# Kernel optimization log

Hardware: AMD Instinct MI355X
Metric: run time of the kernel (lower is better)

The kernel has to match this reference:

```python
import jax, jax.numpy as jnp
import numpy as np

# MX microscaling decode helpers. Codes are stored as int32 holding uint8 bit patterns.
_FP4_MAG = jnp.array([0.0, 0.5, 1.0, 1.5, 2.0, 3.0, 4.0, 6.0], dtype=jnp.float32)  # E2M1

def dec_fp4(c):
    # c in [0,16): bit3 = sign, bits0-2 index E2M1 magnitude LUT
    s = jnp.where(c >= 8, -1.0, 1.0)
    return s * _FP4_MAG[c & 7]

def dec_fp6(c):
    # E3M2, bias 3. bit5 sign, bits2-4 exp, bits0-1 mantissa
    s = jnp.where(c >= 32, -1.0, 1.0)
    e = ((c >> 2) & 7).astype(jnp.float32)
    m = (c & 3).astype(jnp.float32)
    mag = jnp.where(e == 0, m * 0.25 * 0.25, (1.0 + m * 0.25) * jnp.exp2(e - 3.0))
    return s * mag

def dec_fp8(c):
    # E4M3, bias 7. bit7 sign, bits3-6 exp, bits0-2 mantissa (NaN code decoded as 480, consistent both sides)
    s = jnp.where(c >= 128, -1.0, 1.0)
    e = ((c >> 3) & 15).astype(jnp.float32)
    m = (c & 7).astype(jnp.float32)
    mag = jnp.where(e == 0, m * 0.125 * jnp.exp2(-6.0), (1.0 + m * 0.125) * jnp.exp2(e - 7.0))
    return s * mag

def unpack4(p):
    # [..., K//2] bytes -> [..., K] nibbles; low nibble = even element, high = odd
    lo = p & 15
    hi = (p >> 4) & 15
    return jnp.stack([lo, hi], axis=-1).reshape(*p.shape[:-1], p.shape[-1] * 2)

def unpack6(p):
    # little-endian 6-bit packing: 4 values per 3 bytes. [..., K*6//8] -> [..., K]
    g = p.reshape(*p.shape[:-1], -1, 3)
    b0, b1, b2 = g[..., 0], g[..., 1], g[..., 2]
    v0 = b0 & 0x3F
    v1 = ((b0 >> 6) & 3) | ((b1 & 0x0F) << 2)
    v2 = ((b1 >> 4) & 0x0F) | ((b2 & 3) << 4)
    v3 = (b2 >> 2) & 0x3F
    return jnp.stack([v0, v1, v2, v3], axis=-1).reshape(*p.shape[:-1], p.shape[-1] * 4 // 3)

def blockscale(x, sf):
    # x [..., K] fp32, sf [..., K//32] E8M0 exponents: scale = 2^(sf-127) per 32-element block
    scale = jnp.exp2(sf.astype(jnp.float32) - 127.0)
    xs = x.reshape(*x.shape[:-1], -1, 32) * scale[..., None]
    return xs.reshape(x.shape)

def dequant(codes, sf, bits):
    if bits == 4:
        x = dec_fp4(unpack4(codes))
    elif bits == 6:
        x = dec_fp6(unpack6(codes))
    else:
        x = dec_fp8(codes)
    return blockscale(x, sf)


def setup_inputs() -> dict:
    key = jax.random.key(0)
    ks = jax.random.split(key, 13)
    M, N = 4096, 4096
    p4, p6, p8 = 3072, 768, 256
    ri = lambda k, sh: jax.random.randint(k, sh, 0, 256, dtype=jnp.int32)
    sf = lambda k, sh: jax.random.randint(k, sh, 121, 132, dtype=jnp.int32)
    return {
        "AN": ri(ks[0], (M, p4 // 2)),
        "AS": ri(ks[1], (M, p6 * 6 // 8)),
        "AO": ri(ks[2], (M, p8)),
        "SFAN": sf(ks[3], (M, p4 // 32)),
        "SFAS": sf(ks[4], (M, p6 // 32)),
        "SFAO": sf(ks[5], (M, p8 // 32)),
        "BN": ri(ks[6], (N, p4 // 2)),
        "BS": ri(ks[7], (N, p6 * 6 // 8)),
        "BO": ri(ks[8], (N, p8)),
        "SFBN": sf(ks[9], (N * p4 // 32,)),
        "SFBS": sf(ks[10], (N * p6 // 32,)),
        "SFBO": sf(ks[11], (N * p8 // 32,)),
        "bias": jax.random.normal(ks[12], (N,), dtype=jnp.float32) * 0.02,
    }


def reference(AN, AS, AO, SFAN, SFAS, SFAO, BN, BS, BO, SFBN, SFBS, SFBO, bias):
    N = BN.shape[0]
    a4 = dequant(AN, SFAN, 4)                       # [M, p4]
    w4 = dequant(BN, SFBN.reshape(N, -1), 4)        # [N, p4]
    a6 = dequant(AS, SFAS, 6)                       # [M, p6]
    w6 = dequant(BS, SFBS.reshape(N, -1), 6)        # [N, p6]
    a8 = dequant(AO, SFAO, 8)                       # [M, p8]
    w8 = dequant(BO, SFBO.reshape(N, -1), 8)        # [N, p8]
    y = a4 @ w4.T + a6 @ w6.T + a8 @ w8.T           # [M, N]
    return y + bias
```

## Files before the change

kernel.cpp:

```cpp
#include <hip/hip_runtime.h>

typedef short short8 __attribute__((ext_vector_type(8)));
typedef int   intx8  __attribute__((ext_vector_type(8)));
typedef float floatx16 __attribute__((ext_vector_type(16)));

__device__ __forceinline__ unsigned pk4(int a, int b, int c, int d) {
    return (a & 255) | ((b & 255) << 8) | ((c & 255) << 16) | ((unsigned)(d & 255) << 24);
}

__device__ __forceinline__ unsigned dec8bf(int c, int esf) {
    int s = (c & 128) << 8;
    int e = (c >> 3) & 15, m = c & 7;
    int rn = s | ((e + 120 + esf) << 7) | (m << 4);
    int nb = (m >= 4) ? 2 : ((m >= 2) ? 1 : 0);
    int rs = m ? (s | ((nb + 118 + esf) << 7) | ((m << (7 - nb)) & 0x7F)) : s;
    return (unsigned)(e ? rn : rs);
}

__device__ __forceinline__ void pack_one(
    int t, const int* __restrict__ Pn, const int* __restrict__ Ps, const int* __restrict__ Po,
    const int* __restrict__ Sn, const int* __restrict__ Ss, const int* __restrict__ So,
    unsigned char* __restrict__ C4, unsigned char* __restrict__ C6,
    unsigned short* __restrict__ C8, unsigned char* __restrict__ St, int R)
{
    int T0 = R * 384, T1 = T0 + R * 144, T2 = T1 + R * 64, T3 = T2 + R * 24, T4 = T3 + R * 12;
    if (t < T0) {
        int r = t / 384, i = t - r * 384;
        int4 b = *(const int4*)(Pn + (size_t)r * 1536 + i * 4);
        *(unsigned*)(C4 + ((size_t)(i >> 2) * R + r) * 16 + (i & 3) * 4) = pk4(b.x, b.y, b.z, b.w);
    } else if (t < T1) {
        t -= T0; int r = t / 144, i = t - r * 144;
        int4 b = *(const int4*)(Ps + (size_t)r * 576 + i * 4);
        *(unsigned*)(C6 + ((size_t)(i / 6) * R + r) * 24 + (i % 6) * 4) = pk4(b.x, b.y, b.z, b.w);
    } else if (t < T2) {
        t -= T1; int r = t / 64, i = t - r * 64;
        int4 c = *(const int4*)(Po + (size_t)r * 256 + i * 4);
        int e = So[r * 8 + (i >> 3)] - 127;
        unsigned lo = dec8bf(c.x & 255, e) | (dec8bf(c.y & 255, e) << 16);
        unsigned hi = dec8bf(c.z & 255, e) | (dec8bf(c.w & 255, e) << 16);
        *(int2*)((unsigned char*)C8 + ((size_t)(i >> 1) * R + r) * 16 + (i & 1) * 8) =
            (int2){ (int)lo, (int)hi };
    } else if (t < T3) {
        t -= T2; int r = t / 24, q = t - r * 24;
        int4 v = *(const int4*)(Sn + (size_t)r * 96 + q * 4);
        *(unsigned*)(St + ((size_t)q * R + r) * 4) = pk4(v.x, v.y, v.z, v.w);
    } else if (t < T4) {
        t -= T3; int r = t / 12, b2 = t - r * 12;
        int2 sp = *(const int2*)(Ss + (size_t)r * 24 + 2 * b2);
        *(unsigned*)(St + ((size_t)(24 + b2) * R + r) * 4) =
            (unsigned)((sp.x & 255) | ((sp.y & 255) << 8));
    }
}

__global__ __launch_bounds__(256) void pack_both(
    const int* __restrict__ AN, const int* __restrict__ AS, const int* __restrict__ AO,
    const int* __restrict__ SAn, const int* __restrict__ SAs, const int* __restrict__ SAo,
    unsigned char* __restrict__ A4, unsigned char* __restrict__ A6,
    unsigned short* __restrict__ A8, unsigned char* __restrict__ SaT, int M,
    const int* __restrict__ BN, const int* __restrict__ BS, const int* __restrict__ BO,
    const int* __restrict__ SBn, const int* __restrict__ SBs, const int* __restrict__ SBo,
    unsigned char* __restrict__ B4, unsigned char* __restrict__ B6,
    unsigned short* __restrict__ B8, unsigned char* __restrict__ SbT, int N)
{
    int t = blockIdx.x * 256 + threadIdx.x;
    int TA = M * 628;
    if (t < TA) pack_one(t, AN, AS, AO, SAn, SAs, SAo, A4, A6, A8, SaT, M);
    else        pack_one(t - TA, BN, BS, BO, SBn, SBs, SBo, B4, B6, B8, SbT, N);
}

__global__ __launch_bounds__(256, 3) void gemm_mx(
    const unsigned char* __restrict__ A4, const unsigned char* __restrict__ B4,
    const unsigned char* __restrict__ A6, const unsigned char* __restrict__ B6,
    const unsigned short* __restrict__ A8, const unsigned short* __restrict__ B8,
    const unsigned char* __restrict__ SaT, const unsigned char* __restrict__ SbT,
    const float* __restrict__ bias, float* __restrict__ C, int M, int N)
{
    int tid = threadIdx.x, w = tid >> 6, l = tid & 63;
    int nbm = M >> 7, nbn = N >> 7;
    int bm, bn;
    if (nbm == 32 && nbn == 32) {
        int o = blockIdx.y * 32 + blockIdx.x;
        int xcd = o & 7, pos = o >> 3;
        int tile = pos >> 4, idx = pos & 15;
        bm = xcd * 4 + (idx & 3);
        bn = tile * 4 + (idx >> 2);
    } else { bm = blockIdx.y; bn = blockIdx.x; }

    int wm = (w >> 1) * 64, wn = (w & 1) * 64;
    int lr = l & 31, lh = l >> 5;

    floatx16 acc[2][2] = {};

    int rA[2] = { bm * 128 + wm + lr, bm * 128 + wm + 32 + lr };
    int cB[2] = { bn * 128 + wn + lr, bn * 128 + wn + 32 + lr };

    {
        unsigned strA = 32u * (unsigned)M, strB = 32u * (unsigned)N;
        unsigned fA0 = ((unsigned)lh * M + (unsigned)rA[0]) * 16u;
        unsigned fA1 = ((unsigned)lh * M + (unsigned)rA[1]) * 16u;
        unsigned fB0 = ((unsigned)lh * N + (unsigned)cB[0]) * 16u;
        unsigned fB1 = ((unsigned)lh * N + (unsigned)cB[1]) * 16u;

        int4 pa[3][2], pb[3][2];
        #pragma unroll
        for (int s = 0; s < 3; ++s) {
            pa[s][0] = *(const int4*)(A4 + fA0); pa[s][1] = *(const int4*)(A4 + fA1);
            pb[s][0] = *(const int4*)(B4 + fB0); pb[s][1] = *(const int4*)(B4 + fB1);
            fA0 += strA; fA1 += strA; fB0 += strB; fB1 += strB;
        }

        unsigned sstrA = 4u * (unsigned)M, sstrB = 4u * (unsigned)N;
        unsigned sA0 = (unsigned)rA[0] * 4u, sA1 = (unsigned)rA[1] * 4u;
        unsigned sB0 = (unsigned)cB[0] * 4u, sB1 = (unsigned)cB[1] * 4u;
        unsigned psa[2][2], psb[2][2];
        psa[0][0] = *(const unsigned*)(SaT + sA0);         psa[0][1] = *(const unsigned*)(SaT + sA1);
        psb[0][0] = *(const unsigned*)(SbT + sB0);         psb[0][1] = *(const unsigned*)(SbT + sB1);
        psa[1][0] = *(const unsigned*)(SaT + sA0 + sstrA); psa[1][1] = *(const unsigned*)(SaT + sA1 + sstrA);
        psb[1][0] = *(const unsigned*)(SbT + sB0 + sstrB); psb[1][1] = *(const unsigned*)(SbT + sB1 + sstrB);
        sA0 += 2 * sstrA; sA1 += 2 * sstrA; sB0 += 2 * sstrB; sB1 += 2 * sstrB;

        #pragma unroll 12
        for (int u = 0; u < 48; ++u) {
            int sl = u % 3, wsl = (u >> 1) & 1;
            int sh = 8 * ((u & 1) * 2 + lh);
            int sa0 = (int)((psa[wsl][0] >> sh) & 255), sa1 = (int)((psa[wsl][1] >> sh) & 255);
            int sb0 = (int)((psb[wsl][0] >> sh) & 255), sb1 = (int)((psb[wsl][1] >> sh) & 255);
            intx8 A0 = (intx8){ pa[sl][0].x, pa[sl][0].y, pa[sl][0].z, pa[sl][0].w, 0, 0, 0, 0 };
            intx8 A1 = (intx8){ pa[sl][1].x, pa[sl][1].y, pa[sl][1].z, pa[sl][1].w, 0, 0, 0, 0 };
            intx8 B0 = (intx8){ pb[sl][0].x, pb[sl][0].y, pb[sl][0].z, pb[sl][0].w, 0, 0, 0, 0 };
            intx8 B1 = (intx8){ pb[sl][1].x, pb[sl][1].y, pb[sl][1].z, pb[sl][1].w, 0, 0, 0, 0 };
            acc[0][0] = __builtin_amdgcn_mfma_scale_f32_32x32x64_f8f6f4(A0, B0, acc[0][0], 4, 4, 0, sa0, 0, sb0);
            acc[0][1] = __builtin_amdgcn_mfma_scale_f32_32x32x64_f8f6f4(A0, B1, acc[0][1], 4, 4, 0, sa0, 0, sb1);
            acc[1][0] = __builtin_amdgcn_mfma_scale_f32_32x32x64_f8f6f4(A1, B0, acc[1][0], 4, 4, 0, sa1, 0, sb0);
            acc[1][1] = __builtin_amdgcn_mfma_scale_f32_32x32x64_f8f6f4(A1, B1, acc[1][1], 4, 4, 0, sa1, 0, sb1);
            pa[sl][0] = *(const int4*)(A4 + fA0); pa[sl][1] = *(const int4*)(A4 + fA1);
            pb[sl][0] = *(const int4*)(B4 + fB0); pb[sl][1] = *(const int4*)(B4 + fB1);
            fA0 += strA; fA1 += strA; fB0 += strB; fB1 += strB;
            if (u & 1) {
                psa[wsl][0] = *(const unsigned*)(SaT + sA0); psa[wsl][1] = *(const unsigned*)(SaT + sA1);
                psb[wsl][0] = *(const unsigned*)(SbT + sB0); psb[wsl][1] = *(const unsigned*)(SbT + sB1);
                sA0 += sstrA; sA1 += sstrA; sB0 += sstrB; sB1 += sstrB;
            }
        }
    }

    {
        unsigned str6A = 48u * (unsigned)M, str6B = 48u * (unsigned)N;
        unsigned gA0 = ((unsigned)lh * M + (unsigned)rA[0]) * 24u;
        unsigned gA1 = ((unsigned)lh * M + (unsigned)rA[1]) * 24u;
        unsigned gB0 = ((unsigned)lh * N + (unsigned)cB[0]) * 24u;
        unsigned gB1 = ((unsigned)lh * N + (unsigned)cB[1]) * 24u;
        unsigned ss4A = 4u * (unsigned)M, ss4B = 4u * (unsigned)N;
        unsigned zA0 = (24u * (unsigned)M + (unsigned)rA[0]) * 4u;
        unsigned zA1 = (24u * (unsigned)M + (unsigned)rA[1]) * 4u;
        unsigned zB0 = (24u * (unsigned)N + (unsigned)cB[0]) * 4u;
        unsigned zB1 = (24u * (unsigned)N + (unsigned)cB[1]) * 4u;

        int2 qa[2][2][3], qb[2][2][3];
        unsigned p6a[2][2], p6b[2][2];
        #pragma unroll
        for (int s = 0; s < 2; ++s) {
            const unsigned char *a0 = A6 + gA0, *a1 = A6 + gA1, *b0 = B6 + gB0, *b1 = B6 + gB1;
            qa[s][0][0] = *(const int2*)(a0); qa[s][0][1] = *(const int2*)(a0 + 8); qa[s][0][2] = *(const int2*)(a0 + 16);
            qa[s][1][0] = *(const int2*)(a1); qa[s][1][1] = *(const int2*)(a1 + 8); qa[s][1][2] = *(const int2*)(a1 + 16);
            qb[s][0][0] = *(const int2*)(b0); qb[s][0][1] = *(const int2*)(b0 + 8); qb[s][0][2] = *(const int2*)(b0 + 16);
            qb[s][1][0] = *(const int2*)(b1); qb[s][1][1] = *(const int2*)(b1 + 8); qb[s][1][2] = *(const int2*)(b1 + 16);
            p6a[s][0] = *(const unsigned*)(SaT + zA0); p6a[s][1] = *(const unsigned*)(SaT + zA1);
            p6b[s][0] = *(const unsigned*)(SbT + zB0); p6b[s][1] = *(const unsigned*)(SbT + zB1);
            gA0 += str6A; gA1 += str6A; gB0 += str6B; gB1 += str6B;
            zA0 += ss4A; zA1 += ss4A; zB0 += ss4B; zB1 += ss4B;
        }
        int sh6 = 8 * lh;
        #pragma unroll 2
        for (int v = 0; v < 10; ++v) {
            int sl = v & 1;
            int sa0 = (int)((p6a[sl][0] >> sh6) & 255), sa1 = (int)((p6a[sl][1] >> sh6) & 255);
            int sb0 = (int)((p6b[sl][0] >> sh6) & 255), sb1 = (int)((p6b[sl][1] >> sh6) & 255);
            intx8 A0 = (intx8){ qa[sl][0][0].x, qa[sl][0][0].y, qa[sl][0][1].x, qa[sl][0][1].y, qa[sl][0][2].x, qa[sl][0][2].y, 0, 0 };
            intx8 A1 = (intx8){ qa[sl][1][0].x, qa[sl][1][0].y, qa[sl][1][1].x, qa[sl][1][1].y, qa[sl][1][2].x, qa[sl][1][2].y, 0, 0 };
            intx8 B0 = (intx8){ qb[sl][0][0].x, qb[sl][0][0].y, qb[sl][0][1].x, qb[sl][0][1].y, qb[sl][0][2].x, qb[sl][0][2].y, 0, 0 };
            intx8 B1 = (intx8){ qb[sl][1][0].x, qb[sl][1][0].y, qb[sl][1][1].x, qb[sl][1][1].y, qb[sl][1][2].x, qb[sl][1][2].y, 0, 0 };
            acc[0][0] = __builtin_amdgcn_mfma_scale_f32_32x32x64_f8f6f4(A0, B0, acc[0][0], 3, 3, 0, sa0, 0, sb0);
            acc[0][1] = __builtin_amdgcn_mfma_scale_f32_32x32x64_f8f6f4(A0, B1, acc[0][1], 3, 3, 0, sa0, 0, sb1);
            acc[1][0] = __builtin_amdgcn_mfma_scale_f32_32x32x64_f8f6f4(A1, B0, acc[1][0], 3, 3, 0, sa1, 0, sb0);
            acc[1][1] = __builtin_amdgcn_mfma_scale_f32_32x32x64_f8f6f4(A1, B1, acc[1][1], 3, 3, 0, sa1, 0, sb1);
            {
                const unsigned char *a0 = A6 + gA0, *a1 = A6 + gA1, *b0 = B6 + gB0, *b1 = B6 + gB1;
                qa[sl][0][0] = *(const int2*)(a0); qa[sl][0][1] = *(const int2*)(a0 + 8); qa[sl][0][2] = *(const int2*)(a0 + 16);
                qa[sl][1][0] = *(const int2*)(a1); qa[sl][1][1] = *(const int2*)(a1 + 8); qa[sl][1][2] = *(const int2*)(a1 + 16);
                qb[sl][0][0] = *(const int2*)(b0); qb[sl][0][1] = *(const int2*)(b0 + 8); qb[sl][0][2] = *(const int2*)(b0 + 16);
                qb[sl][1][0] = *(const int2*)(b1); qb[sl][1][1] = *(const int2*)(b1 + 8); qb[sl][1][2] = *(const int2*)(b1 + 16);
                p6a[sl][0] = *(const unsigned*)(SaT + zA0); p6a[sl][1] = *(const unsigned*)(SaT + zA1);
                p6b[sl][0] = *(const unsigned*)(SbT + zB0); p6b[sl][1] = *(const unsigned*)(SbT + zB1);
                gA0 += str6A; gA1 += str6A; gB0 += str6B; gB1 += str6B;
                zA0 += ss4A; zA1 += ss4A; zB0 += ss4B; zB1 += ss4B;
            }
        }
        #pragma unroll
        for (int v = 10; v < 12; ++v) {
            int sl = v & 1;
            int sa0 = (int)((p6a[sl][0] >> sh6) & 255), sa1 = (int)((p6a[sl][1] >> sh6) & 255);
            int sb0 = (int)((p6b[sl][0] >> sh6) & 255), sb1 = (int)((p6b[sl][1] >> sh6) & 255);
            intx8 A0 = (intx8){ qa[sl][0][0].x, qa[sl][0][0].y, qa[sl][0][1].x, qa[sl][0][1].y, qa[sl][0][2].x, qa[sl][0][2].y, 0, 0 };
            intx8 A1 = (intx8){ qa[sl][1][0].x, qa[sl][1][0].y, qa[sl][1][1].x, qa[sl][1][1].y, qa[sl][1][2].x, qa[sl][1][2].y, 0, 0 };
            intx8 B0 = (intx8){ qb[sl][0][0].x, qb[sl][0][0].y, qb[sl][0][1].x, qb[sl][0][1].y, qb[sl][0][2].x, qb[sl][0][2].y, 0, 0 };
            intx8 B1 = (intx8){ qb[sl][1][0].x, qb[sl][1][0].y, qb[sl][1][1].x, qb[sl][1][1].y, qb[sl][1][2].x, qb[sl][1][2].y, 0, 0 };
            acc[0][0] = __builtin_amdgcn_mfma_scale_f32_32x32x64_f8f6f4(A0, B0, acc[0][0], 3, 3, 0, sa0, 0, sb0);
            acc[0][1] = __builtin_amdgcn_mfma_scale_f32_32x32x64_f8f6f4(A0, B1, acc[0][1], 3, 3, 0, sa0, 0, sb1);
            acc[1][0] = __builtin_amdgcn_mfma_scale_f32_32x32x64_f8f6f4(A1, B0, acc[1][0], 3, 3, 0, sa1, 0, sb0);
            acc[1][1] = __builtin_amdgcn_mfma_scale_f32_32x32x64_f8f6f4(A1, B1, acc[1][1], 3, 3, 0, sa1, 0, sb1);
        }
    }

    {
        unsigned str8A = 32u * (unsigned)M, str8B = 32u * (unsigned)N;
        const unsigned char* A8b = (const unsigned char*)A8;
        const unsigned char* B8b = (const unsigned char*)B8;
        unsigned hA0 = ((unsigned)lh * M + (unsigned)rA[0]) * 16u;
        unsigned hA1 = ((unsigned)lh * M + (unsigned)rA[1]) * 16u;
        unsigned hB0 = ((unsigned)lh * N + (unsigned)cB[0]) * 16u;
        unsigned hB1 = ((unsigned)lh * N + (unsigned)cB[1]) * 16u;
        short8 ra[2][2], rb[2][2];
        #pragma unroll
        for (int s = 0; s < 2; ++s) {
            ra[s][0] = *(const short8*)(A8b + hA0); ra[s][1] = *(const short8*)(A8b + hA1);
            rb[s][0] = *(const short8*)(B8b + hB0); rb[s][1] = *(const short8*)(B8b + hB1);
            hA0 += str8A; hA1 += str8A; hB0 += str8B; hB1 += str8B;
        }
        #pragma unroll 2
        for (int q = 0; q < 16; ++q) {
            int sl = q & 1;
            acc[0][0] = __builtin_amdgcn_mfma_f32_32x32x16_bf16(ra[sl][0], rb[sl][0], acc[0][0], 0, 0, 0);
            acc[0][1] = __builtin_amdgcn_mfma_f32_32x32x16_bf16(ra[sl][0], rb[sl][1], acc[0][1], 0, 0, 0);
            acc[1][0] = __builtin_amdgcn_mfma_f32_32x32x16_bf16(ra[sl][1], rb[sl][0], acc[1][0], 0, 0, 0);
            acc[1][1] = __builtin_amdgcn_mfma_f32_32x32x16_bf16(ra[sl][1], rb[sl][1], acc[1][1], 0, 0, 0);
            ra[sl][0] = *(const short8*)(A8b + hA0); ra[sl][1] = *(const short8*)(A8b + hA1);
            rb[sl][0] = *(const short8*)(B8b + hB0); rb[sl][1] = *(const short8*)(B8b + hB1);
            hA0 += str8A; hA1 += str8A; hB0 += str8B; hB1 += str8B;
        }
    }

    #pragma unroll
    for (int i = 0; i < 2; i++)
        #pragma unroll
        for (int j = 0; j < 2; j++) {
            int col = bn * 128 + wn + j * 32 + lr;
            float bv = bias[col];
            #pragma unroll
            for (int r = 0; r < 16; r++) {
                int row = bm * 128 + wm + i * 32 + (r & 3) + 8 * (r >> 2) + 4 * lh;
                C[(size_t)row * N + col] = acc[i][j][r] + bv;
            }
        }
}

extern "C" void kernel_launch(void* const* d_in, const int* in_sizes, int n_in,
                              void* d_out, int out_size, void* d_ws, size_t ws_size,
                              hipStream_t stream) {
    const int* AN   = (const int*)d_in[0];
    const int* ASs  = (const int*)d_in[1];
    const int* AO   = (const int*)d_in[2];
    const int* SFAN = (const int*)d_in[3];
    const int* SFAS = (const int*)d_in[4];
    const int* SFAO = (const int*)d_in[5];
    const int* BN   = (const int*)d_in[6];
    const int* BS   = (const int*)d_in[7];
    const int* BO   = (const int*)d_in[8];
    const int* SFBN = (const int*)d_in[9];
    const int* SFBS = (const int*)d_in[10];
    const int* SFBO = (const int*)d_in[11];
    const float* bias = (const float*)d_in[12];

    int M = in_sizes[0] / 1536;
    int N = in_sizes[6] / 1536;

    unsigned char* ws = (unsigned char*)d_ws;
    size_t o = 0;
    unsigned char*  A4c = ws + o;                    o += (size_t)M * 1536;
    unsigned char*  B4c = ws + o;                    o += (size_t)N * 1536;
    unsigned char*  A6c = ws + o;                    o += (size_t)M * 576;
    unsigned char*  B6c = ws + o;                    o += (size_t)N * 576;
    unsigned short* A8d = (unsigned short*)(ws + o); o += (size_t)M * 512;
    unsigned short* B8d = (unsigned short*)(ws + o); o += (size_t)N * 512;
    unsigned char*  SaT = ws + o;                    o += (size_t)36 * M * 4;
    unsigned char*  SbT = ws + o;                    o += (size_t)36 * N * 4;

    int T = M * 628 + N * 628;
    pack_both<<<(T + 255) / 256, 256, 0, stream>>>(
        AN, ASs, AO, SFAN, SFAS, SFAO, A4c, A6c, A8d, SaT, M,
        BN, BS, BO, SFBN, SFBS, SFBO, B4c, B6c, B8d, SbT, N);

    dim3 grid(N / 128, M / 128);
    gemm_mx<<<grid, 256, 0, stream>>>(A4c, B4c, A6c, B6c, A8d, B8d,
                                      SaT, SbT, bias, (float*)d_out, M, N);
}
```

Before: 230.6 us.

## Stage pack transposes through LDS and deepen GEMM fp4 prefetch to four stages

Replaces the per-thread scattered pack kernel with a block-tiled version that stages 64 rows in shared memory, then writes the column-major repacked layout with wide coalesced stores. A and B are now packed in two separate launches. The GEMM's fp4 register prefetch ring grows from three to four stages, the unroll drops to 4, and the occupancy hint drops from 3 to 2 blocks. This trades occupancy for more memory-latency hiding, and adds an extra kernel launch plus LDS usage in the pack step.

```diff
diff --git a/kernel.cpp b/kernel.cpp
--- a/kernel.cpp
+++ b/kernel.cpp
@@ -17,58 +17,95 @@
     return (unsigned)(e ? rn : rs);
 }
 
-__device__ __forceinline__ void pack_one(
-    int t, const int* __restrict__ Pn, const int* __restrict__ Ps, const int* __restrict__ Po,
+__global__ __launch_bounds__(256) void pack_lds(
+    const int* __restrict__ Pn, const int* __restrict__ Ps, const int* __restrict__ Po,
     const int* __restrict__ Sn, const int* __restrict__ Ss, const int* __restrict__ So,
     unsigned char* __restrict__ C4, unsigned char* __restrict__ C6,
     unsigned short* __restrict__ C8, unsigned char* __restrict__ St, int R)
 {
-    int T0 = R * 384, T1 = T0 + R * 144, T2 = T1 + R * 64, T3 = T2 + R * 24, T4 = T3 + R * 12;
-    if (t < T0) {
-        int r = t / 384, i = t - r * 384;
-        int4 b = *(const int4*)(Pn + (size_t)r * 1536 + i * 4);
-        *(unsigned*)(C4 + ((size_t)(i >> 2) * R + r) * 16 + (i & 3) * 4) = pk4(b.x, b.y, b.z, b.w);
-    } else if (t < T1) {
-        t -= T0; int r = t / 144, i = t - r * 144;
-        int4 b = *(const int4*)(Ps + (size_t)r * 576 + i * 4);
-        *(unsigned*)(C6 + ((size_t)(i / 6) * R + r) * 24 + (i % 6) * 4) = pk4(b.x, b.y, b.z, b.w);
-    } else if (t < T2) {
-        t -= T1; int r = t / 64, i = t - r * 64;
-        int4 c = *(const int4*)(Po + (size_t)r * 256 + i * 4);
-        int e = So[r * 8 + (i >> 3)] - 127;
-        unsigned lo = dec8bf(c.x & 255, e) | (dec8bf(c.y & 255, e) << 16);
-        unsigned hi = dec8bf(c.z & 255, e) | (dec8bf(c.w & 255, e) << 16);
-        *(int2*)((unsigned char*)C8 + ((size_t)(i >> 1) * R + r) * 16 + (i & 1) * 8) =
-            (int2){ (int)lo, (int)hi };
-    } else if (t < T3) {
-        t -= T2; int r = t / 24, q = t - r * 24;
-        int4 v = *(const int4*)(Sn + (size_t)r * 96 + q * 4);
-        *(unsigned*)(St + ((size_t)q * R + r) * 4) = pk4(v.x, v.y, v.z, v.w);
-    } else if (t < T4) {
-        t -= T3; int r = t / 12, b2 = t - r * 12;
-        int2 sp = *(const int2*)(Ss + (size_t)r * 24 + 2 * b2);
-        *(unsigned*)(St + ((size_t)(24 + b2) * R + r) * 4) =
-            (unsigned)((sp.x & 255) | ((sp.y & 255) << 8));
+    __shared__ unsigned lds[9216];
+    int t = threadIdx.x, b = blockIdx.x, per = R >> 6;
+    if (b < 4 * per) {
+        int jg = b / per, rb = b - jg * per, r0 = rb << 6;
+        #pragma unroll
+        for (int i = 0; i < 24; ++i) {
+            int idx = i * 256 + t, row = idx / 96, q4 = idx - row * 96;
+            int4 v = *(const int4*)(Pn + (size_t)(r0 + row) * 1536 + jg * 384 + q4 * 4);
+            lds[row * 96 + q4] = pk4(v.x, v.y, v.z, v.w);
+        }
+        __syncthreads();
+        #pragma unroll
+        for (int i = 0; i < 6; ++i) {
+            int idx = i * 256 + t, j = idx >> 6, row = idx & 63;
+            uint4 v = *(uint4*)&lds[row * 96 + j * 4];
+            *(uint4*)(C4 + ((size_t)(jg * 24 + j) * R + r0 + row) * 16) = v;
+        }
+    } else if (b < 5 * per) {
+        int rb = b - 4 * per, r0 = rb << 6;
+        #pragma unroll
+        for (int i = 0; i < 36; ++i) {
+            int idx = i * 256 + t, row = idx / 144, q4 = idx - row * 144;
+            int4 v = *(const int4*)(Ps + (size_t)(r0 + row) * 576 + q4 * 4);
+            lds[row * 144 + q4] = pk4(v.x, v.y, v.z, v.w);
+        }
+        __syncthreads();
+        #pragma unroll
+        for (int i = 0; i < 18; ++i) {
+            int idx = i * 256 + t, seg = idx / 192, off = idx - seg * 192;
+            int row = off / 3, m3 = off - row * 3;
+            int w0 = row * 144 + seg * 6 + m3 * 2;
+            int2 v = { (int)lds[w0], (int)lds[w0 + 1] };
+            *(int2*)(C6 + ((size_t)seg * R + r0) * 24 + (size_t)off * 8) = v;
+        }
+    } else if (b < 6 * per) {
+        int rb = b - 5 * per, r0 = rb << 6;
+        #pragma unroll
+        for (int i = 0; i < 16; ++i) {
+            int idx = i * 256 + t, row = idx >> 6, q4 = idx & 63;
+            int4 c = *(const int4*)(Po + (size_t)(r0 + row) * 256 + q4 * 4);
+            int e = So[(size_t)(r0 + row) * 8 + (q4 >> 3)] - 127;
+            lds[row * 128 + q4 * 2]     = dec8bf(c.x & 255, e) | (dec8bf(c.y & 255, e) << 16);
+            lds[row * 128 + q4 * 2 + 1] = dec8bf(c.z & 255, e) | (dec8bf(c.w & 255, e) << 16);
+        }
+        __syncthreads();
+        #pragma unroll
+        for (int i = 0; i < 8; ++i) {
+            int idx = i * 256 + t, seg = idx >> 6, row = idx & 63;
+            uint4 v = *(uint4*)&lds[row * 128 + seg * 4];
+            *(uint4*)((unsigned char*)C8 + ((size_t)seg * R + r0 + row) * 16) = v;
+        }
+    } else if (b < 7 * per) {
+        int rb = b - 6 * per, r0 = rb << 6;
+        #pragma unroll
+        for (int i = 0; i < 6; ++i) {
+            int idx = i * 256 + t, row = idx / 24, q4 = idx - row * 24;
+            int4 v = *(const int4*)(Sn + (size_t)(r0 + row) * 96 + q4 * 4);
+            lds[row * 24 + q4] = pk4(v.x, v.y, v.z, v.w);
+        }
+        __syncthreads();
+        #pragma unroll
+        for (int i = 0; i < 6; ++i) {
+            int idx = i * 256 + t, seg = idx >> 6, row = idx & 63;
+            *(unsigned*)(St + ((size_t)seg * R + r0 + row) * 4) = lds[row * 24 + seg];
+        }
+    } else {
+        int rb = b - 7 * per, r0 = rb << 6;
+        #pragma unroll
+        for (int i = 0; i < 3; ++i) {
+            int idx = i * 256 + t, row = idx / 12, b2 = idx - row * 12;
+            int2 v = *(const int2*)(Ss + (size_t)(r0 + row) * 24 + b2 * 2);
+            lds[row * 12 + b2] = (unsigned)((v.x & 255) | ((v.y & 255) << 8));
+        }
+        __syncthreads();
+        #pragma unroll
+        for (int i = 0; i < 3; ++i) {
+            int idx = i * 256 + t, seg = idx >> 6, row = idx & 63;
+            *(unsigned*)(St + ((size_t)(24 + seg) * R + r0 + row) * 4) = lds[row * 12 + seg];
+        }
     }
 }
 
-__global__ __launch_bounds__(256) void pack_both(
-    const int* __restrict__ AN, const int* __restrict__ AS, const int* __restrict__ AO,
-    const int* __restrict__ SAn, const int* __restrict__ SAs, const int* __restrict__ SAo,
-    unsigned char* __restrict__ A4, unsigned char* __restrict__ A6,
-    unsigned short* __restrict__ A8, unsigned char* __restrict__ SaT, int M,
-    const int* __restrict__ BN, const int* __restrict__ BS, const int* __restrict__ BO,
-    const int* __restrict__ SBn, const int* __restrict__ SBs, const int* __restrict__ SBo,
-    unsigned char* __restrict__ B4, unsigned char* __restrict__ B6,
-    unsigned short* __restrict__ B8, unsigned char* __restrict__ SbT, int N)
-{
-    int t = blockIdx.x * 256 + threadIdx.x;
-    int TA = M * 628;
-    if (t < TA) pack_one(t, AN, AS, AO, SAn, SAs, SAo, A4, A6, A8, SaT, M);
-    else        pack_one(t - TA, BN, BS, BO, SBn, SBs, SBo, B4, B6, B8, SbT, N);
-}
-
-__global__ __launch_bounds__(256, 3) void gemm_mx(
+__global__ __launch_bounds__(256, 2) void gemm_mx(
     const unsigned char* __restrict__ A4, const unsigned char* __restrict__ B4,
     const unsigned char* __restrict__ A6, const unsigned char* __restrict__ B6,
     const unsigned short* __restrict__ A8, const unsigned short* __restrict__ B8,
@@ -101,9 +138,9 @@
         unsigned fB0 = ((unsigned)lh * N + (unsigned)cB[0]) * 16u;
         unsigned fB1 = ((unsigned)lh * N + (unsigned)cB[1]) * 16u;
 
-        int4 pa[3][2], pb[3][2];
-        #pragma unroll
-        for (int s = 0; s < 3; ++s) {
+        int4 pa[4][2], pb[4][2];
+        #pragma unroll
+        for (int s = 0; s < 4; ++s) {
             pa[s][0] = *(const int4*)(A4 + fA0); pa[s][1] = *(const int4*)(A4 + fA1);
             pb[s][0] = *(const int4*)(B4 + fB0); pb[s][1] = *(const int4*)(B4 + fB1);
             fA0 += strA; fA1 += strA; fB0 += strB; fB1 += strB;
@@ -119,9 +156,9 @@
         psb[1][0] = *(const unsigned*)(SbT + sB0 + sstrB); psb[1][1] = *(const unsigned*)(SbT + sB1 + sstrB);
         sA0 += 2 * sstrA; sA1 += 2 * sstrA; sB0 += 2 * sstrB; sB1 += 2 * sstrB;
 
-        #pragma unroll 12
+        #pragma unroll 4
         for (int u = 0; u < 48; ++u) {
-            int sl = u % 3, wsl = (u >> 1) & 1;
+            int sl = u & 3, wsl = (u >> 1) & 1;
             int sh = 8 * ((u & 1) * 2 + lh);
             int sa0 = (int)((psa[wsl][0] >> sh) & 255), sa1 = (int)((psa[wsl][1] >> sh) & 255);
             int sb0 = (int)((psb[wsl][0] >> sh) & 255), sb1 = (int)((psb[wsl][1] >> sh) & 255);
@@ -285,10 +322,10 @@
     unsigned char*  SaT = ws + o;                    o += (size_t)36 * M * 4;
     unsigned char*  SbT = ws + o;                    o += (size_t)36 * N * 4;
 
-    int T = M * 628 + N * 628;
-    pack_both<<<(T + 255) / 256, 256, 0, stream>>>(
-        AN, ASs, AO, SFAN, SFAS, SFAO, A4c, A6c, A8d, SaT, M,
-        BN, BS, BO, SFBN, SFBS, SFBO, B4c, B6c, B8d, SbT, N);
+    pack_lds<<<(M >> 6) * 8, 256, 0, stream>>>(AN, ASs, AO, SFAN, SFAS, SFAO,
+                                               A4c, A6c, A8d, SaT, M);
+    pack_lds<<<(N >> 6) * 8, 256, 0, stream>>>(BN, BS, BO, SFBN, SFBS, SFBO,
+                                               B4c, B6c, B8d, SbT, N);
 
     dim3 grid(N / 128, M / 128);
     gemm_mx<<<grid, 256, 0, stream>>>(A4c, B4c, A6c, B6c, A8d, B8d,
```

Measured after the change: 220.1 us. 4.6% less time.
